# Optimization experiments

Measured on AMD Instinct MI355X. Metric: run time of the kernel, lower is better.

## Reference

```python
import jax, jax.numpy as jnp
import numpy as np
from jax import lax

EPS = 1e-6


def layernorm2d(x, w, b):
    # channel LayerNorm over dim C of NCHW (biased variance), matching LayerNormFunction
    mu = jnp.mean(x, axis=1, keepdims=True)
    var = jnp.mean((x - mu) ** 2, axis=1, keepdims=True)
    y = (x - mu) * lax.rsqrt(var + EPS)
    return w[None, :, None, None] * y + b[None, :, None, None]


def conv1x1(x, W, b):
    # x: (N,C,H,W), W: (O,C), b: (O,)
    return jnp.einsum('nchw,oc->nohw', x, W) + b[None, :, None, None]


def conv3x3(x, W, b):
    # W: (O,I,3,3)
    y = lax.conv_general_dilated(x, W, window_strides=(1, 1), padding='SAME',
                                 dimension_numbers=('NCHW', 'OIHW', 'NCHW'))
    return y + b[None, :, None, None]


def avg_pool3x3(x):
    # torch F.avg_pool2d k=3, s=1, p=1, count_include_pad=True -> always divide by 9
    s = lax.reduce_window(x, 0.0, lax.add, (1, 1, 3, 3), (1, 1, 1, 1),
                          [(0, 0), (0, 0), (1, 1), (1, 1)])
    return s / 9.0


def setup_inputs() -> dict:
    key = jax.random.key(0)
    N, C, H, W = 8, 64, 128, 256
    ks = jax.random.split(key, 12)
    d = {
        'x_l': jax.random.normal(ks[0], (N, C, H, W), jnp.float32),
        'x_r': jax.random.normal(ks[1], (N, C, H, W), jnp.float32),
        'nl_w': jnp.ones((C,), jnp.float32),
        'nl_b': jnp.zeros((C,), jnp.float32),
        'nr_w': jnp.ones((C,), jnp.float32),
        'nr_b': jnp.zeros((C,), jnp.float32),
        'Wq_l': jax.random.normal(ks[2], (C, C), jnp.float32) * 0.05,
        'bq_l': jax.random.normal(ks[3], (C,), jnp.float32) * 0.05,
        'Wq_r': jax.random.normal(ks[4], (C, C), jnp.float32) * 0.05,
        'bq_r': jax.random.normal(ks[5], (C,), jnp.float32) * 0.05,
        'Wv_r': jax.random.normal(ks[6], (C, C), jnp.float32) * 0.05,
        'bv_r': jax.random.normal(ks[7], (C,), jnp.float32) * 0.05,
        'beta': jax.random.normal(ks[8], (1, C, 1, 1), jnp.float32) * 0.1,
        'gamma': jax.random.normal(ks[9], (1, C, 1, 1), jnp.float32) * 0.1,
        'W_hf': jax.random.normal(ks[10], (C, C, 3, 3), jnp.float32) * 0.02,
        'b_hf': jax.random.normal(ks[11], (C,), jnp.float32) * 0.02,
    }
    return d


def reference(x_l, x_r, nl_w, nl_b, nr_w, nr_b, Wq_l, bq_l, Wq_r, bq_r,
              Wv_r, bv_r, beta, gamma, W_hf, b_hf):
    C = x_l.shape[1]
    scale = C ** (-0.5)

    # Projections (1x1 convs); Q_l, Q_r, V_r as (N,H,W,C)
    Q_l = jnp.transpose(conv1x1(layernorm2d(x_l, nl_w, nl_b), Wq_l, bq_l), (0, 2, 3, 1))
    Q_r = jnp.transpose(conv1x1(layernorm2d(x_r, nr_w, nr_b), Wq_r, bq_r), (0, 2, 3, 1))
    V_r = jnp.transpose(conv1x1(x_r, Wv_r, bv_r), (0, 2, 3, 1))

    # Per-scanline cross attention: (N,H,W,W)
    attn = jnp.einsum('nhwc,nhvc->nhwv', Q_l, Q_r) * scale
    attn = jax.nn.softmax(attn, axis=-1)
    F_r2l = jnp.einsum('nhwv,nhvc->nhwc', attn, V_r)  # (N,H,W,C)
    F_r2l = jnp.transpose(F_r2l, (0, 3, 1, 2)) * beta  # (N,C,H,W)

    # High-frequency branch
    hf = conv3x3(x_r - avg_pool3x3(x_r), W_hf, b_hf)

    return x_l + F_r2l + gamma * hf
```

## Files before the change

kernel.cpp:

```cpp
#include <hip/hip_runtime.h>
#include <hip/hip_bf16.h>

#define N_ 8
#define C_ 64
#define H_ 128
#define W_ 256
#define HW_ (H_*W_)
#define CHW_ (C_*H_*W_)

typedef unsigned int u32;
typedef unsigned short u16;
typedef float f32x4 __attribute__((ext_vector_type(4)));
typedef short bf16x8 __attribute__((ext_vector_type(8)));

__device__ __forceinline__ float blo(u32 u) { return __uint_as_float(u << 16); }
__device__ __forceinline__ float bhi(u32 u) { return __uint_as_float(u & 0xffff0000u); }
__device__ __forceinline__ u16 f2bf(float f) {
    u32 u = __float_as_uint(f);
    u32 lsb = (u >> 16) & 1u;
    u += 0x7fffu + lsb;
    return (u16)(u >> 16);
}
__device__ __forceinline__ u32 pack2(float a, float b) {
    return (u32)f2bf(a) | ((u32)f2bf(b) << 16);
}
__device__ __forceinline__ int rmap(int px) {
    return (px & 0xF8) | ((px + (px >> 3)) & 7);
}

__global__ __launch_bounds__(256) void k_proj(
    const float* __restrict__ xl, const float* __restrict__ xr,
    const float* __restrict__ nlw, const float* __restrict__ nlb,
    const float* __restrict__ nrw, const float* __restrict__ nrb,
    const float* __restrict__ Wql, const float* __restrict__ bql,
    const float* __restrict__ Wqr, const float* __restrict__ bqr,
    const float* __restrict__ Wvr, const float* __restrict__ bvr,
    u32* __restrict__ Ql, u32* __restrict__ Qr, u32* __restrict__ Vr)
{
    __shared__ u32 Xs32[256*32];
    __shared__ float muA[256], rsA[256];
    __shared__ float SlA[64], BlA[64], SrA[64], BrA[64], BvA[64];
    const int tid  = threadIdx.x;
    const int lane = tid & 63, wv = tid >> 6;
    const int l15  = lane & 15, kg = lane >> 4;
    const int blk  = blockIdx.x;
    const int n = blk >> 7, h = blk & 127;
    const size_t gbase = (size_t)n*CHW_ + (size_t)h*W_;
    const size_t rowb  = (size_t)blk*256;

    if (tid < 64) {
        const int o = tid;
        float sl = 0.f, bl = bql[o], sr = 0.f, br = bqr[o];
        for (int c = 0; c < 64; ++c) {
            float wl = Wql[o*64+c], wr = Wqr[o*64+c];
            sl += wl * nlw[c];
            bl += wl * nlb[c];
            sr += wr * nrw[c];
            br += wr * nrb[c];
        }
        SlA[o] = sl; BlA[o] = bl; SrA[o] = sr; BrA[o] = br; BvA[o] = bvr[o];
    }

    const int oA = wv*16 + l15;
    bf16x8 aL[2], aR[2], aV[2];
    #pragma unroll
    for (int hf = 0; hf < 2; ++hf) {
        bf16x8 tl, tr, tv;
        #pragma unroll
        for (int j = 0; j < 8; ++j) {
            const int c = hf*32 + kg*8 + j;
            tl[j] = (short)f2bf(Wql[oA*64+c] * nlw[c]);
            tr[j] = (short)f2bf(Wqr[oA*64+c] * nrw[c]);
            tv[j] = (short)f2bf(Wvr[oA*64+c]);
        }
        aL[hf] = tl; aR[hf] = tr; aV[hf] = tv;
    }

    #pragma unroll
    for (int it2 = 0; it2 < 2; ++it2) {
        const int g = it2*256 + tid;
        const int chunk = g >> 6;
        const int j = g & 63;
        const int c0 = chunk*8;
        float4 v[8];
        #pragma unroll
        for (int e = 0; e < 8; ++e)
            v[e] = *(const float4*)(xl + gbase + (size_t)(c0+e)*HW_ + j*4);
        #pragma unroll
        for (int t = 0; t < 4; ++t) {
            const int px = j*4 + t;
            const int r = rmap(px);
            u32 q0,q1,q2,q3;
            const float* f0 = (const float*)&v[0]; const float* f1 = (const float*)&v[1];
            const float* f2 = (const float*)&v[2]; const float* f3 = (const float*)&v[3];
            const float* f4 = (const float*)&v[4]; const float* f5 = (const float*)&v[5];
            const float* f6 = (const float*)&v[6]; const float* f7 = (const float*)&v[7];
            asm("v_cvt_pk_bf16_f32 %0, %1, %2" : "=v"(q0) : "v"(f0[t]), "v"(f1[t]));
            asm("v_cvt_pk_bf16_f32 %0, %1, %2" : "=v"(q1) : "v"(f2[t]), "v"(f3[t]));
            asm("v_cvt_pk_bf16_f32 %0, %1, %2" : "=v"(q2) : "v"(f4[t]), "v"(f5[t]));
            asm("v_cvt_pk_bf16_f32 %0, %1, %2" : "=v"(q3) : "v"(f6[t]), "v"(f7[t]));
            uint4 pv; pv.x=q0; pv.y=q1; pv.z=q2; pv.w=q3;
            *(uint4*)&Xs32[r*32 + ((chunk ^ (r&7))<<2)] = pv;
        }
    }
    __syncthreads();
    {
        const int px = tid & 255;
        const int r = rmap(px);
        float sum = 0.f, ssq = 0.f;
        #pragma unroll
        for (int c8 = 0; c8 < 8; ++c8) {
            uint4 val = *(const uint4*)&Xs32[r*32 + ((c8 ^ (r&7))<<2)];
            const u32* wp = (const u32*)&val;
            #pragma unroll
            for (int q = 0; q < 4; ++q) {
                float a = blo(wp[q]), b = bhi(wp[q]);
                sum += a + b; ssq += a*a + b*b;
            }
        }
        float mu = sum * (1.f/64.f);
        float var = ssq * (1.f/64.f) - mu*mu;
        muA[px] = mu;
        rsA[px] = rsqrtf(var + 1e-6f);
    }
    __syncthreads();
    {
        float Sv[4], Bv[4];
        #pragma unroll
        for (int r4 = 0; r4 < 4; ++r4) {
            Sv[r4] = SlA[wv*16 + kg*4 + r4];
            Bv[r4] = BlA[wv*16 + kg*4 + r4];
        }
        #pragma unroll
        for (int nt = 0; nt < 16; ++nt) {
            const int px = nt*16 + l15;
            const int r = rmap(px);
            f32x4 d = {0.f,0.f,0.f,0.f};
            #pragma unroll
            for (int hf = 0; hf < 2; ++hf) {
                bf16x8 b = *(const bf16x8*)&Xs32[r*32 + (((hf*4+kg) ^ (r&7))<<2)];
                d = __builtin_amdgcn_mfma_f32_16x16x32_bf16(aL[hf], b, d, 0, 0, 0);
            }
            const float mu = muA[px], rs = rsA[px];
            uint2 pv;
            pv.x = pack2(rs*(d[0] - mu*Sv[0]) + Bv[0], rs*(d[1] - mu*Sv[1]) + Bv[1]);
            pv.y = pack2(rs*(d[2] - mu*Sv[2]) + Bv[2], rs*(d[3] - mu*Sv[3]) + Bv[3]);
            *(uint2*)&Ql[(rowb + px)*32 + wv*8 + kg*2] = pv;
        }
    }
    __syncthreads();

    #pragma unroll
    for (int it2 = 0; it2 < 2; ++it2) {
        const int g = it2*256 + tid;
        const int chunk = g >> 6;
        const int j = g & 63;
        const int c0 = chunk*8;
        float4 v[8];
        #pragma unroll
        for (int e = 0; e < 8; ++e)
            v[e] = *(const float4*)(xr + gbase + (size_t)(c0+e)*HW_ + j*4);
        #pragma unroll
        for (int t = 0; t < 4; ++t) {
            const int px = j*4 + t;
            const int r = rmap(px);
            u32 q0,q1,q2,q3;
            const float* f0 = (const float*)&v[0]; const float* f1 = (const float*)&v[1];
            const float* f2 = (const float*)&v[2]; const float* f3 = (const float*)&v[3];
            const float* f4 = (const float*)&v[4]; const float* f5 = (const float*)&v[5];
            const float* f6 = (const float*)&v[6]; const float* f7 = (const float*)&v[7];
            asm("v_cvt_pk_bf16_f32 %0, %1, %2" : "=v"(q0) : "v"(f0[t]), "v"(f1[t]));
            asm("v_cvt_pk_bf16_f32 %0, %1, %2" : "=v"(q1) : "v"(f2[t]), "v"(f3[t]));
            asm("v_cvt_pk_bf16_f32 %0, %1, %2" : "=v"(q2) : "v"(f4[t]), "v"(f5[t]));
            asm("v_cvt_pk_bf16_f32 %0, %1, %2" : "=v"(q3) : "v"(f6[t]), "v"(f7[t]));
            uint4 pv; pv.x=q0; pv.y=q1; pv.z=q2; pv.w=q3;
            *(uint4*)&Xs32[r*32 + ((chunk ^ (r&7))<<2)] = pv;
        }
    }
    __syncthreads();
    {
        const int px = tid & 255;
        const int r = rmap(px);
        float sum = 0.f, ssq = 0.f;
        #pragma unroll
        for (int c8 = 0; c8 < 8; ++c8) {
            uint4 val = *(const uint4*)&Xs32[r*32 + ((c8 ^ (r&7))<<2)];
            const u32* wp = (const u32*)&val;
            #pragma unroll
            for (int q = 0; q < 4; ++q) {
                float a = blo(wp[q]), b = bhi(wp[q]);
                sum += a + b; ssq += a*a + b*b;
            }
        }
        float mu = sum * (1.f/64.f);
        float var = ssq * (1.f/64.f) - mu*mu;
        muA[px] = mu;
        rsA[px] = rsqrtf(var + 1e-6f);
    }
    __syncthreads();
    {
        float Sv[4], Bv[4], Vb[4];
        #pragma unroll
        for (int r4 = 0; r4 < 4; ++r4) {
            Sv[r4] = SrA[wv*16 + kg*4 + r4];
            Bv[r4] = BrA[wv*16 + kg*4 + r4];
            Vb[r4] = BvA[wv*16 + kg*4 + r4];
        }
        #pragma unroll
        for (int nt = 0; nt < 16; ++nt) {
            const int px = nt*16 + l15;
            const int r = rmap(px);
            f32x4 dq = {0.f,0.f,0.f,0.f};
            f32x4 dv = {0.f,0.f,0.f,0.f};
            #pragma unroll
            for (int hf = 0; hf < 2; ++hf) {
                bf16x8 b = *(const bf16x8*)&Xs32[r*32 + (((hf*4+kg) ^ (r&7))<<2)];
                dq = __builtin_amdgcn_mfma_f32_16x16x32_bf16(aR[hf], b, dq, 0, 0, 0);
                dv = __builtin_amdgcn_mfma_f32_16x16x32_bf16(aV[hf], b, dv, 0, 0, 0);
            }
            const float mu = muA[px], rs = rsA[px];
            uint2 pq, pw;
            pq.x = pack2(rs*(dq[0] - mu*Sv[0]) + Bv[0], rs*(dq[1] - mu*Sv[1]) + Bv[1]);
            pq.y = pack2(rs*(dq[2] - mu*Sv[2]) + Bv[2], rs*(dq[3] - mu*Sv[3]) + Bv[3]);
            pw.x = pack2(dv[0] + Vb[0], dv[1] + Vb[1]);
            pw.y = pack2(dv[2] + Vb[2], dv[3] + Vb[3]);
            *(uint2*)&Qr[(rowb + px)*32 + wv*8 + kg*2] = pq;
            *(uint2*)&Vr[(rowb + px)*32 + wv*8 + kg*2] = pw;
        }
    }
}

__global__ __launch_bounds__(256, 2) void k_attn(
    const u32* __restrict__ Ql, const u32* __restrict__ Qr, const u32* __restrict__ Vr,
    const float* __restrict__ xl, const float* __restrict__ beta,
    float* __restrict__ out)
{
    __shared__ uint4 Ks[2048];
    __shared__ u16  Vts[16384];
    __shared__ u32  Pscr[4096];
    const int tid  = threadIdx.x;
    const int lane = tid & 63, wv = tid >> 6;
    const int l15  = lane & 15, kg = lane >> 4;
    const int blk  = blockIdx.x;
    const int n = blk >> 7, h = blk & 127;
    const size_t rowb = (size_t)blk*256;

    for (int it = tid; it < 2048; it += 256) {
        int key = it >> 3, c = it & 7;
        uint4 v = *(const uint4*)(Qr + (rowb + key)*32 + c*4);
        Ks[key*8 + (c ^ (key & 7))] = v;
    }
    for (int it = tid; it < 2048; it += 256) {
        int key = it & 255, j = it >> 8;
        uint4 v = *(const uint4*)(Vr + (rowb + key)*32 + j*4);
        const u32* vw = (const u32*)&v;
        #pragma unroll
        for (int t = 0; t < 8; ++t) {
            int ch = j*8 + t;
            u32 wd = vw[t >> 1];
            u16 hv = (t & 1) ? (u16)(wd >> 16) : (u16)(wd & 0xffffu);
            Vts[ch*256 + ((key >> 3) ^ (ch & 7))*8 + (key & 7)] = hv;
        }
    }

    const int q0 = wv*64;
    bf16x8 qf[4][2];
    #pragma unroll
    for (int nt = 0; nt < 4; ++nt)
        #pragma unroll
        for (int ci = 0; ci < 2; ++ci)
            qf[nt][ci] = *(const bf16x8*)(Ql + (rowb + q0 + nt*16 + l15)*32 + ci*16 + kg*4);

    f32x4 oacc[4][4];
    #pragma unroll
    for (int a = 0; a < 4; ++a)
        #pragma unroll
        for (int b = 0; b < 4; ++b)
            oacc[a][b] = (f32x4){0.f,0.f,0.f,0.f};
    float lsum[4] = {0.f,0.f,0.f,0.f};
    u32* Pw = &Pscr[wv*1024];

    __syncthreads();

    for (int kb = 0; kb < 8; ++kb) {
        f32x4 st[2][4];
        #pragma unroll
        for (int mt = 0; mt < 2; ++mt)
            #pragma unroll
            for (int nt = 0; nt < 4; ++nt)
                st[mt][nt] = (f32x4){0.f,0.f,0.f,0.f};
        #pragma unroll
        for (int ci = 0; ci < 2; ++ci) {
            bf16x8 a0 = *(const bf16x8*)&Ks[(kb*32 +      l15)*8 + ((ci*4 + kg) ^ (l15 & 7))];
            bf16x8 a1 = *(const bf16x8*)&Ks[(kb*32 + 16 + l15)*8 + ((ci*4 + kg) ^ (l15 & 7))];
            #pragma unroll
            for (int nt = 0; nt < 4; ++nt) {
                st[0][nt] = __builtin_amdgcn_mfma_f32_16x16x32_bf16(a0, qf[nt][ci], st[0][nt], 0, 0, 0);
                st[1][nt] = __builtin_amdgcn_mfma_f32_16x16x32_bf16(a1, qf[nt][ci], st[1][nt], 0, 0, 0);
            }
        }
        #pragma unroll
        for (int nt = 0; nt < 4; ++nt) {
            const int q = nt*16 + l15;
            #pragma unroll
            for (int mt = 0; mt < 2; ++mt) {
                float p0 = __expf(st[mt][nt][0]*0.125f);
                float p1 = __expf(st[mt][nt][1]*0.125f);
                float p2 = __expf(st[mt][nt][2]*0.125f);
                float p3 = __expf(st[mt][nt][3]*0.125f);
                lsum[nt] += (p0+p1)+(p2+p3);
                u32 pr0, pr1;
                asm("v_cvt_pk_bf16_f32 %0, %1, %2" : "=v"(pr0) : "v"(p0), "v"(p1));
                asm("v_cvt_pk_bf16_f32 %0, %1, %2" : "=v"(pr1) : "v"(p2), "v"(p3));
                const int c16 = (2*mt + (kg >> 1)) ^ (q & 3);
                uint2 pv; pv.x = pr0; pv.y = pr1;
                *(uint2*)&Pw[q*16 + c16*4 + (kg & 1)*2] = pv;
            }
        }
        asm volatile("s_waitcnt lgkmcnt(0)" ::: "memory");
        bf16x8 vb[4];
        #pragma unroll
        for (int nc = 0; nc < 4; ++nc)
            vb[nc] = *(const bf16x8*)&Vts[(nc*16 + l15)*256 + ((kb*4 + kg) ^ (l15 & 7))*8];
        #pragma unroll
        for (int qt = 0; qt < 4; ++qt) {
            const int q = qt*16 + l15;
            bf16x8 pa = *(const bf16x8*)&Pw[q*16 + (kg ^ (q & 3))*4];
            #pragma unroll
            for (int nc = 0; nc < 4; ++nc)
                oacc[qt][nc] = __builtin_amdgcn_mfma_f32_16x16x32_bf16(pa, vb[nc], oacc[qt][nc], 0, 0, 0);
        }
    }

    #pragma unroll
    for (int nt = 0; nt < 4; ++nt) {
        float s = lsum[nt];
        s += __shfl_xor(s, 16, 64);
        s += __shfl_xor(s, 32, 64);
        lsum[nt] = s;
    }
    float linv[4][4];
    #pragma unroll
    for (int qt = 0; qt < 4; ++qt)
        #pragma unroll
        for (int r = 0; r < 4; ++r)
            linv[qt][r] = 1.0f / __shfl(lsum[qt], kg*4 + r, 64);

    float* PwF = (float*)Pw;
    const size_t obase = (size_t)n*CHW_ + (size_t)h*W_ + q0;
    #pragma unroll
    for (int nc = 0; nc < 4; ++nc) {
        asm volatile("s_waitcnt lgkmcnt(0)" ::: "memory");
        #pragma unroll
        for (int qt = 0; qt < 4; ++qt) {
            f32x4 vals;
            vals[0] = oacc[qt][nc][0]*linv[qt][0];
            vals[1] = oacc[qt][nc][1]*linv[qt][1];
            vals[2] = oacc[qt][nc][2]*linv[qt][2];
            vals[3] = oacc[qt][nc][3]*linv[qt][3];
            *(f32x4*)&PwF[l15*64 + ((qt*4 + kg) ^ l15)*4] = vals;
        }
        asm volatile("s_waitcnt lgkmcnt(0)" ::: "memory");
        #pragma unroll
        for (int chl = 0; chl < 16; ++chl) {
            const int ch = nc*16 + chl;
            float v = PwF[chl*64 + ((lane >> 2) ^ chl)*4 + (lane & 3)];
            size_t gidx = obase + (size_t)ch*HW_ + lane;
            float prev = out[gidx];
            out[gidx] = xl[gidx] + beta[ch]*v + prev;
        }
    }
}

__global__ __launch_bounds__(256) void k_hipass(
    const float* __restrict__ xr, u16* __restrict__ Tt)
{
    __shared__ u16 Ts[64*256];
    const int bid = blockIdx.x;
    const int blk = (bid & 7)*128 + (bid >> 3);
    const int n = blk >> 7, h = blk & 127;
    const int tid = threadIdx.x;
    const int lane = tid & 63, wv = tid >> 6;
    const float* rowp = xr + (size_t)n*CHW_ + (size_t)h*W_ + lane*4;

    #pragma unroll
    for (int ci = 0; ci < 16; ++ci) {
        const int c = wv*16 + ci;
        const float* pc = rowp + (size_t)c*HW_;
        float ctr0=0.f, ctr1=0.f, ctr2=0.f, ctr3=0.f;
        float s0=0.f, s1=0.f, s2=0.f, s3=0.f;
        #pragma unroll
        for (int dy = -1; dy <= 1; ++dy) {
            const int hh = h + dy;
            float4 v = {0.f,0.f,0.f,0.f};
            if (hh >= 0 && hh < 128) v = *(const float4*)(pc + dy*W_);
            float lft = __shfl_up(v.w, 1);
            float rgt = __shfl_down(v.x, 1);
            if (lane == 0)  lft = 0.f;
            if (lane == 63) rgt = 0.f;
            s0 += lft + v.x + v.y;
            s1 += v.x + v.y + v.z;
            s2 += v.y + v.z + v.w;
            s3 += v.z + v.w + rgt;
            if (dy == 0) { ctr0=v.x; ctr1=v.y; ctr2=v.z; ctr3=v.w; }
        }
        uint2 pv;
        pv.x = pack2(ctr0 - s0*(1.f/9.f), ctr1 - s1*(1.f/9.f));
        pv.y = pack2(ctr2 - s2*(1.f/9.f), ctr3 - s3*(1.f/9.f));
        const int swz = (c >> 3) << 3;
        *(uint2*)&Ts[c*256 + ((lane*4) ^ swz)] = pv;
    }
    __syncthreads();
    uint4* gout = (uint4*)(Tt + (size_t)blk*256*64);
    #pragma unroll
    for (int iter = 0; iter < 8; ++iter) {
        const int lin = iter*256 + tid;
        const int px = lin >> 3, chunk = lin & 7;
        const int pxs = px ^ (chunk << 3);
        u32 w4[4];
        #pragma unroll
        for (int tp = 0; tp < 4; ++tp) {
            const int c0 = chunk*8 + tp*2;
            u16 a = Ts[(c0    )*256 + pxs];
            u16 b = Ts[(c0 + 1)*256 + pxs];
            w4[tp] = (u32)a | ((u32)b << 16);
        }
        uint4 v; v.x=w4[0]; v.y=w4[1]; v.z=w4[2]; v.w=w4[3];
        gout[lin] = v;
    }
}

__device__ __forceinline__ void conv_tile(
    const uint4* __restrict__ buf, const bf16x8* A,
    const float* gv, const float* bv,
    int n, int h, int w0, int mt, int l15, int kg,
    float* __restrict__ out)
{
    f32x4 acc[4] = {{0,0,0,0},{0,0,0,0},{0,0,0,0},{0,0,0,0}};
    #pragma unroll
    for (int s = 0; s < 18; ++s) {
        const int q  = s >> 1;
        const int dy = q / 3, dx = q % 3;
        const int c0 = (s & 1)*4 + kg;
        #pragma unroll
        for (int nt = 0; nt < 4; ++nt) {
            const int wt = nt*16 + l15 + dx;
            bf16x8 b = *(const bf16x8*)&buf[(dy*66 + wt)*8 + (c0 ^ (wt & 7))];
            acc[nt] = __builtin_amdgcn_mfma_f32_16x16x32_bf16(A[s], b, acc[nt], 0, 0, 0);
        }
    }
    #pragma unroll
    for (int nt = 0; nt < 4; ++nt) {
        const int px = w0 + nt*16 + l15;
        #pragma unroll
        for (int r = 0; r < 4; ++r) {
            const int oo = mt*16 + kg*4 + r;
            size_t idx = (size_t)(n*64 + oo)*HW_ + (size_t)h*W_ + px;
            out[idx] = gv[r]*(acc[nt][r] + bv[r]);
        }
    }
}

__global__ __launch_bounds__(256) void k_conv(
    const u16* __restrict__ Tt, const float* __restrict__ Whf,
    const float* __restrict__ bhf, const float* __restrict__ gam,
    float* __restrict__ out)
{
    __shared__ uint4 Xs[2][1584];
    const int tid  = threadIdx.x;
    const int lane = tid & 63;
    const int mt   = tid >> 6;
    const int l15  = lane & 15;
    const int kg   = lane >> 4;
    const int bid  = blockIdx.x;
    const int blk2 = (bid & 7)*256 + (bid >> 3);
    const int row  = blk2 >> 1, half = blk2 & 1;
    const int n = row >> 7, h = row & 127;
    const int w00 = half*128;
    const int w01 = w00 + 64;

    const int oa = mt*16 + l15;
    bf16x8 A[18];
    #pragma unroll
    for (int s = 0; s < 18; ++s) {
        const int q  = s >> 1;
        const int ib = (s & 1)*32 + kg*8;
        bf16x8 a;
        #pragma unroll
        for (int j = 0; j < 8; ++j) {
            float wv = Whf[(size_t)(oa*64 + ib + j)*9 + q];
            a[j] = (short)f2bf(wv);
        }
        A[s] = a;
    }
    float gv[4], bv[4];
    #pragma unroll
    for (int r = 0; r < 4; ++r) {
        int oo = mt*16 + kg*4 + r;
        gv[r] = gam[oo];
        bv[r] = bhf[oo];
    }

    for (int it = tid; it < 1584; it += 256) {
        int dy    = it / 528;
        int rem   = it - dy*528;
        int wt    = rem >> 3;
        int chunk = rem & 7;
        int hh = h + dy - 1;
        int wg = w00 + wt - 1;
        uint4 v = {0,0,0,0};
        if (hh >= 0 && hh < 128 && wg >= 0 && wg < 256)
            v = *(const uint4*)(Tt + (((size_t)(n*128 + hh)*256 + wg)*64 + chunk*8));
        Xs[0][(dy*66 + wt)*8 + (chunk ^ (wt & 7))] = v;
    }
    __syncthreads();

    uint4 rr[7];
    #pragma unroll
    for (int k = 0; k < 7; ++k) {
        const int it = k*256 + tid;
        if (it < 1584) {
            int dy    = it / 528;
            int rem   = it - dy*528;
            int wt    = rem >> 3;
            int chunk = rem & 7;
            int hh = h + dy - 1;
            int wg = w01 + wt - 1;
            uint4 v = {0,0,0,0};
            if (hh >= 0 && hh < 128 && wg >= 0 && wg < 256)
                v = *(const uint4*)(Tt + (((size_t)(n*128 + hh)*256 + wg)*64 + chunk*8));
            rr[k] = v;
        }
    }

    conv_tile(&Xs[0][0], A, gv, bv, n, h, w00, mt, l15, kg, out);

    #pragma unroll
    for (int k = 0; k < 7; ++k) {
        const int it = k*256 + tid;
        if (it < 1584) {
            int dy    = it / 528;
            int rem   = it - dy*528;
            int wt    = rem >> 3;
            int chunk = rem & 7;
            Xs[1][(dy*66 + wt)*8 + (chunk ^ (wt & 7))] = rr[k];
        }
    }
    __syncthreads();
    conv_tile(&Xs[1][0], A, gv, bv, n, h, w01, mt, l15, kg, out);
}

extern "C" void kernel_launch(void* const* d_in, const int* in_sizes, int n_in,
                              void* d_out, int out_size, void* d_ws, size_t ws_size,
                              hipStream_t stream)
{
    const float* xl   = (const float*)d_in[0];
    const float* xr   = (const float*)d_in[1];
    const float* nlw  = (const float*)d_in[2];
    const float* nlb  = (const float*)d_in[3];
    const float* nrw  = (const float*)d_in[4];
    const float* nrb  = (const float*)d_in[5];
    const float* Wql  = (const float*)d_in[6];
    const float* bql  = (const float*)d_in[7];
    const float* Wqr  = (const float*)d_in[8];
    const float* bqr  = (const float*)d_in[9];
    const float* Wvr  = (const float*)d_in[10];
    const float* bvr  = (const float*)d_in[11];
    const float* beta = (const float*)d_in[12];
    const float* gam  = (const float*)d_in[13];
    const float* Whf  = (const float*)d_in[14];
    const float* bhf  = (const float*)d_in[15];
    float* out = (float*)d_out;

    u32* Ql = (u32*)d_ws;
    u32* Qr = Ql + 8388608;
    u32* Vr = Qr + 8388608;
    u16* Tt = (u16*)(Vr + 8388608);

    k_proj<<<1024, 256, 0, stream>>>(xl, xr, nlw, nlb, nrw, nrb,
                                     Wql, bql, Wqr, bqr, Wvr, bvr, Ql, Qr, Vr);
    k_hipass<<<1024, 256, 0, stream>>>(xr, Tt);
    k_conv<<<2048, 256, 0, stream>>>(Tt, Whf, bhf, gam, out);
    k_attn<<<1024, 256, 0, stream>>>(Ql, Qr, Vr, xl, beta, out);
}
```

Before: 215.5 us.

## Fuse projection kernel into attention kernel, keeping Q/K/V in LDS

Merges the LayerNorm+1x1 projection kernel with the per-scanline attention kernel so that Q_l, Q_r and V_r are produced directly into shared memory in the layouts attention expects, including a transposed V computed by swapping MFMA operands. This removes the global write and re-read of three bf16 intermediate tensors and one kernel launch. The cost is a larger LDS footprint per block (two 32KB buffers plus the K buffer), which may reduce occupancy compared with the old __launch_bounds__(256,2) attention kernel. It also loses the overlap that came from splitting the work across separate kernels.

```diff
diff --git a/kernel.cpp b/kernel.cpp
--- a/kernel.cpp
+++ b/kernel.cpp
@@ -28,16 +28,18 @@
     return (px & 0xF8) | ((px + (px >> 3)) & 7);
 }
 
-__global__ __launch_bounds__(256) void k_proj(
+__global__ __launch_bounds__(256) void k_fused(
     const float* __restrict__ xl, const float* __restrict__ xr,
     const float* __restrict__ nlw, const float* __restrict__ nlb,
     const float* __restrict__ nrw, const float* __restrict__ nrb,
     const float* __restrict__ Wql, const float* __restrict__ bql,
     const float* __restrict__ Wqr, const float* __restrict__ bqr,
     const float* __restrict__ Wvr, const float* __restrict__ bvr,
-    u32* __restrict__ Ql, u32* __restrict__ Qr, u32* __restrict__ Vr)
+    const float* __restrict__ beta, float* __restrict__ out)
 {
-    __shared__ u32 Xs32[256*32];
+    __shared__ u32 B1[8192];
+    __shared__ u32 B2[8192];
+    __shared__ uint4 Ks[2048];
     __shared__ float muA[256], rsA[256];
     __shared__ float SlA[64], BlA[64], SrA[64], BrA[64], BvA[64];
     const int tid  = threadIdx.x;
@@ -46,7 +48,6 @@
     const int blk  = blockIdx.x;
     const int n = blk >> 7, h = blk & 127;
     const size_t gbase = (size_t)n*CHW_ + (size_t)h*W_;
-    const size_t rowb  = (size_t)blk*256;
 
     if (tid < 64) {
         const int o = tid;
@@ -100,7 +101,7 @@
             asm("v_cvt_pk_bf16_f32 %0, %1, %2" : "=v"(q2) : "v"(f4[t]), "v"(f5[t]));
             asm("v_cvt_pk_bf16_f32 %0, %1, %2" : "=v"(q3) : "v"(f6[t]), "v"(f7[t]));
             uint4 pv; pv.x=q0; pv.y=q1; pv.z=q2; pv.w=q3;
-            *(uint4*)&Xs32[r*32 + ((chunk ^ (r&7))<<2)] = pv;
+            *(uint4*)&B1[r*32 + ((chunk ^ (r&7))<<2)] = pv;
         }
     }
     __syncthreads();
@@ -110,7 +111,7 @@
         float sum = 0.f, ssq = 0.f;
         #pragma unroll
         for (int c8 = 0; c8 < 8; ++c8) {
-            uint4 val = *(const uint4*)&Xs32[r*32 + ((c8 ^ (r&7))<<2)];
+            uint4 val = *(const uint4*)&B1[r*32 + ((c8 ^ (r&7))<<2)];
             const u32* wp = (const u32*)&val;
             #pragma unroll
             for (int q = 0; q < 4; ++q) {
@@ -138,18 +139,27 @@
             f32x4 d = {0.f,0.f,0.f,0.f};
             #pragma unroll
             for (int hf = 0; hf < 2; ++hf) {
-                bf16x8 b = *(const bf16x8*)&Xs32[r*32 + (((hf*4+kg) ^ (r&7))<<2)];
+                bf16x8 b = *(const bf16x8*)&B1[r*32 + (((hf*4+kg) ^ (r&7))<<2)];
                 d = __builtin_amdgcn_mfma_f32_16x16x32_bf16(aL[hf], b, d, 0, 0, 0);
             }
             const float mu = muA[px], rs = rsA[px];
             uint2 pv;
             pv.x = pack2(rs*(d[0] - mu*Sv[0]) + Bv[0], rs*(d[1] - mu*Sv[1]) + Bv[1]);
             pv.y = pack2(rs*(d[2] - mu*Sv[2]) + Bv[2], rs*(d[3] - mu*Sv[3]) + Bv[3]);
-            *(uint2*)&Ql[(rowb + px)*32 + wv*8 + kg*2] = pv;
-        }
-    }
-    __syncthreads();
-
+            const int ci = (wv*2 + (kg>>1)) ^ (px & 7);
+            *(uint2*)&B2[px*32 + (ci<<2) + (kg&1)*2] = pv;
+        }
+    }
+    __syncthreads();
+
+    bf16x8 qf[4][2];
+    #pragma unroll
+    for (int ntq = 0; ntq < 4; ++ntq)
+        #pragma unroll
+        for (int ci = 0; ci < 2; ++ci) {
+            const int q = wv*64 + ntq*16 + l15;
+            qf[ntq][ci] = *(const bf16x8*)&B2[q*32 + (((ci*4+kg) ^ (q&7))<<2)];
+        }
     #pragma unroll
     for (int it2 = 0; it2 < 2; ++it2) {
         const int g = it2*256 + tid;
@@ -174,7 +184,7 @@
             asm("v_cvt_pk_bf16_f32 %0, %1, %2" : "=v"(q2) : "v"(f4[t]), "v"(f5[t]));
             asm("v_cvt_pk_bf16_f32 %0, %1, %2" : "=v"(q3) : "v"(f6[t]), "v"(f7[t]));
             uint4 pv; pv.x=q0; pv.y=q1; pv.z=q2; pv.w=q3;
-            *(uint4*)&Xs32[r*32 + ((chunk ^ (r&7))<<2)] = pv;
+            *(uint4*)&B1[r*32 + ((chunk ^ (r&7))<<2)] = pv;
         }
     }
     __syncthreads();
@@ -184,7 +194,7 @@
         float sum = 0.f, ssq = 0.f;
         #pragma unroll
         for (int c8 = 0; c8 < 8; ++c8) {
-            uint4 val = *(const uint4*)&Xs32[r*32 + ((c8 ^ (r&7))<<2)];
+            uint4 val = *(const uint4*)&B1[r*32 + ((c8 ^ (r&7))<<2)];
             const u32* wp = (const u32*)&val;
             #pragma unroll
             for (int q = 0; q < 4; ++q) {
@@ -199,77 +209,45 @@
     }
     __syncthreads();
     {
-        float Sv[4], Bv[4], Vb[4];
+        float Sv[4], Bv[4];
         #pragma unroll
         for (int r4 = 0; r4 < 4; ++r4) {
             Sv[r4] = SrA[wv*16 + kg*4 + r4];
             Bv[r4] = BrA[wv*16 + kg*4 + r4];
-            Vb[r4] = BvA[wv*16 + kg*4 + r4];
-        }
+        }
+        const int chv = wv*16 + l15;
+        const float vbias = BvA[chv];
+        u32* KsW = (u32*)Ks;
+        u16* Vts = (u16*)B2;
         #pragma unroll
         for (int nt = 0; nt < 16; ++nt) {
             const int px = nt*16 + l15;
             const int r = rmap(px);
+            bf16x8 bX[2];
+            #pragma unroll
+            for (int hf = 0; hf < 2; ++hf)
+                bX[hf] = *(const bf16x8*)&B1[r*32 + (((hf*4+kg) ^ (r&7))<<2)];
             f32x4 dq = {0.f,0.f,0.f,0.f};
             f32x4 dv = {0.f,0.f,0.f,0.f};
             #pragma unroll
             for (int hf = 0; hf < 2; ++hf) {
-                bf16x8 b = *(const bf16x8*)&Xs32[r*32 + (((hf*4+kg) ^ (r&7))<<2)];
-                dq = __builtin_amdgcn_mfma_f32_16x16x32_bf16(aR[hf], b, dq, 0, 0, 0);
-                dv = __builtin_amdgcn_mfma_f32_16x16x32_bf16(aV[hf], b, dv, 0, 0, 0);
+                dq = __builtin_amdgcn_mfma_f32_16x16x32_bf16(aR[hf], bX[hf], dq, 0, 0, 0);
+                dv = __builtin_amdgcn_mfma_f32_16x16x32_bf16(bX[hf], aV[hf], dv, 0, 0, 0);
             }
             const float mu = muA[px], rs = rsA[px];
-            uint2 pq, pw;
+            uint2 pq;
             pq.x = pack2(rs*(dq[0] - mu*Sv[0]) + Bv[0], rs*(dq[1] - mu*Sv[1]) + Bv[1]);
             pq.y = pack2(rs*(dq[2] - mu*Sv[2]) + Bv[2], rs*(dq[3] - mu*Sv[3]) + Bv[3]);
-            pw.x = pack2(dv[0] + Vb[0], dv[1] + Vb[1]);
-            pw.y = pack2(dv[2] + Vb[2], dv[3] + Vb[3]);
-            *(uint2*)&Qr[(rowb + px)*32 + wv*8 + kg*2] = pq;
-            *(uint2*)&Vr[(rowb + px)*32 + wv*8 + kg*2] = pw;
-        }
-    }
-}
-
-__global__ __launch_bounds__(256, 2) void k_attn(
-    const u32* __restrict__ Ql, const u32* __restrict__ Qr, const u32* __restrict__ Vr,
-    const float* __restrict__ xl, const float* __restrict__ beta,
-    float* __restrict__ out)
-{
-    __shared__ uint4 Ks[2048];
-    __shared__ u16  Vts[16384];
-    __shared__ u32  Pscr[4096];
-    const int tid  = threadIdx.x;
-    const int lane = tid & 63, wv = tid >> 6;
-    const int l15  = lane & 15, kg = lane >> 4;
-    const int blk  = blockIdx.x;
-    const int n = blk >> 7, h = blk & 127;
-    const size_t rowb = (size_t)blk*256;
-
-    for (int it = tid; it < 2048; it += 256) {
-        int key = it >> 3, c = it & 7;
-        uint4 v = *(const uint4*)(Qr + (rowb + key)*32 + c*4);
-        Ks[key*8 + (c ^ (key & 7))] = v;
-    }
-    for (int it = tid; it < 2048; it += 256) {
-        int key = it & 255, j = it >> 8;
-        uint4 v = *(const uint4*)(Vr + (rowb + key)*32 + j*4);
-        const u32* vw = (const u32*)&v;
-        #pragma unroll
-        for (int t = 0; t < 8; ++t) {
-            int ch = j*8 + t;
-            u32 wd = vw[t >> 1];
-            u16 hv = (t & 1) ? (u16)(wd >> 16) : (u16)(wd & 0xffffu);
-            Vts[ch*256 + ((key >> 3) ^ (ch & 7))*8 + (key & 7)] = hv;
-        }
-    }
-
-    const int q0 = wv*64;
-    bf16x8 qf[4][2];
-    #pragma unroll
-    for (int nt = 0; nt < 4; ++nt)
-        #pragma unroll
-        for (int ci = 0; ci < 2; ++ci)
-            qf[nt][ci] = *(const bf16x8*)(Ql + (rowb + q0 + nt*16 + l15)*32 + ci*16 + kg*4);
+            const int ciq = (wv*2 + (kg>>1)) ^ (px & 7);
+            *(uint2*)&KsW[px*32 + (ciq<<2) + (kg&1)*2] = pq;
+            uint2 pw;
+            pw.x = pack2(dv[0] + vbias, dv[1] + vbias);
+            pw.y = pack2(dv[2] + vbias, dv[3] + vbias);
+            const int swz = (nt*2 + (kg>>1)) ^ (chv & 7);
+            *(uint2*)&Vts[chv*256 + (swz<<3) + (kg&1)*4] = pw;
+        }
+    }
+    __syncthreads();
 
     f32x4 oacc[4][4];
     #pragma unroll
@@ -278,9 +256,9 @@
         for (int b = 0; b < 4; ++b)
             oacc[a][b] = (f32x4){0.f,0.f,0.f,0.f};
     float lsum[4] = {0.f,0.f,0.f,0.f};
-    u32* Pw = &Pscr[wv*1024];
-
-    __syncthreads();
+    u32* Pw = &B1[wv*1024];
+    const u16* Vts = (const u16*)B2;
+    const int q0 = wv*64;
 
     for (int kb = 0; kb < 8; ++kb) {
         f32x4 st[2][4];
@@ -572,14 +550,11 @@
     const float* bhf  = (const float*)d_in[15];
     float* out = (float*)d_out;
 
-    u32* Ql = (u32*)d_ws;
-    u32* Qr = Ql + 8388608;
-    u32* Vr = Qr + 8388608;
-    u16* Tt = (u16*)(Vr + 8388608);
-
-    k_proj<<<1024, 256, 0, stream>>>(xl, xr, nlw, nlb, nrw, nrb,
-                                     Wql, bql, Wqr, bqr, Wvr, bvr, Ql, Qr, Vr);
+    u16* Tt = (u16*)d_ws;
+
     k_hipass<<<1024, 256, 0, stream>>>(xr, Tt);
     k_conv<<<2048, 256, 0, stream>>>(Tt, Whf, bhf, gam, out);
-    k_attn<<<1024, 256, 0, stream>>>(Ql, Qr, Vr, xl, beta, out);
-}
+    k_fused<<<1024, 256, 0, stream>>>(xl, xr, nlw, nlb, nrw, nrb,
+                                      Wql, bql, Wqr, bqr, Wvr, bvr,
+                                      beta, out);
+}
```

Result: faster. 194.3 us (-9.8%).
